# Performance work log

Hardware: AMD Instinct MI355X
Metric: run time of the kernel (lower is better)

## Reference

```python
import jax, jax.numpy as jnp
import numpy as np

KR = 2  # nb_row == stride_row
KC = 2  # nb_col == stride_col


def setup_inputs() -> dict:
    key = jax.random.key(0)
    k1, k2, k3 = jax.random.split(key, 3)
    B, C, H, W_ = 32, 32, 128, 128
    F = 64
    OR, OC = H // KR, W_ // KC
    x = jax.random.normal(k1, (B, C, H, W_), dtype=jnp.float32)
    W = jax.random.normal(k2, (F, C, H, W_), dtype=jnp.float32) * 0.05
    b = jax.random.normal(k3, (OR, OC, F), dtype=jnp.float32) * 0.05
    return {"x": x, "W": W, "b": b}


def reference(x, W, b):
    # x: (B, C, H, W), W: (F, C, H, W) -- unshared per-pixel weights
    # per-pixel channel contraction: (B, F, H, W)
    out = jnp.einsum('bchw,fchw->bfhw', x, W)
    B, F, H, Wd = out.shape
    OR, OC = H // KR, Wd // KC
    # stride*avg_pool == exact sum over non-overlapping (KR, KC) patches
    out = out.reshape(B, F, OR, KR, OC, KC).sum(axis=(3, 5))
    # keras does a RAW reshape of b from (OR, OC, F) to (1, F, OR, OC)
    out = out + b.reshape(1, F, OR, OC)
    return jax.nn.relu(out)
```

## Files before the change

kernel.cpp:

```cpp
#include <hip/hip_runtime.h>
#include <stdint.h>


#define CC  32
#define HH  128
#define WWD 128
#define FF  64
#define ORR 64
#define OCC 64
#define NIT 32
#define HW  (HH * WWD)
#define CHW (CC * HH * WWD)

__global__ __launch_bounds__(512, 4) void lc2d_kernel(
    const float* __restrict__ x, const float* __restrict__ wgt,
    const float* __restrict__ bias, float* __restrict__ out)
{
    __shared__ __align__(16) float Xs[4][2048];
    __shared__ __align__(16) float Ws[4][2048];

    const int tid  = threadIdx.x;
    const int id   = blockIdx.x;
    const int fblk = id >> 8;
    const int low  = id & 255;
    const int oct = ((low & 1) << 1) | (low >> 7);
    const int orr = (low >> 1) & 63;
    const int w0  = oct * 32;
    const int h0  = orr * 2;

    const int lane = tid & 63;
    const int wv   = tid >> 6;
    const int chk  = lane & 7;
    const int sub  = lane >> 3;

    const int skh = wv >> 2;
    const int bsw = sub * 4 + (wv & 3);
    const int flr = (wv & 3) * 8 + sub;
    const float* gx = x   + (((bsw * CC) * HH) + h0 + skh) * WWD + w0 + chk * 4;
    const float* gw = wgt + ((((fblk * 32 + flr) * CC) * HH) + h0 + skh) * WWD + w0 + chk * 4;

    auto issue = [&](int p) {
        __builtin_amdgcn_global_load_lds(
            (const __attribute__((address_space(1))) void*)gx,
            (__attribute__((address_space(3))) void*)(&Xs[p][wv * 256]), 16, 0, 0);
        __builtin_amdgcn_global_load_lds(
            (const __attribute__((address_space(1))) void*)gw,
            (__attribute__((address_space(3))) void*)(&Ws[p][wv * 256]), 16, 0, 0);
        gx += HW; gw += HW;
    };

    const int ocg = tid & 7;
    const int bg  = (tid >> 3) & 7;
    const int woff = wv * 128 + ocg * 4;

    float acc0[4][4], acc1[4][4];
#pragma unroll
    for (int i = 0; i < 4; ++i)
#pragma unroll
        for (int q = 0; q < 4; ++q) { acc0[i][q] = 0.f; acc1[i][q] = 0.f; }

    issue(0); issue(1); issue(2); issue(3);

    for (int it = 0; it < NIT; ++it) {
        const int rem = NIT - 1 - it;
        if (rem >= 3)      asm volatile("s_waitcnt vmcnt(6)");
        else if (rem == 2) asm volatile("s_waitcnt vmcnt(4)");
        else if (rem == 1) asm volatile("s_waitcnt vmcnt(2)");
        else               asm volatile("s_waitcnt vmcnt(0)");
        __builtin_amdgcn_sched_barrier(0);
        __builtin_amdgcn_s_barrier();
        __builtin_amdgcn_sched_barrier(0);

        const int p = it & 3;
        const float* Xp = Xs[p];
        const float* Wp = Ws[p];
#pragma unroll
        for (int s = 0; s < 2; ++s) {
            const float4* xr = (const float4*)(Xp + s * 1024 + (lane << 2));
            const float4* wr = (const float4*)(Wp + s * 1024 + woff);
            float4 xa[4], wb[4];
#pragma unroll
            for (int i = 0; i < 4; ++i) xa[i] = xr[i * 64];
#pragma unroll
            for (int q = 0; q < 4; ++q) wb[q] = wr[q * 8];
#pragma unroll
            for (int i = 0; i < 4; ++i)
#pragma unroll
                for (int q = 0; q < 4; ++q) {
                    acc0[i][q] = fmaf(xa[i].x, wb[q].x, acc0[i][q]);
                    acc0[i][q] = fmaf(xa[i].y, wb[q].y, acc0[i][q]);
                    acc1[i][q] = fmaf(xa[i].z, wb[q].z, acc1[i][q]);
                    acc1[i][q] = fmaf(xa[i].w, wb[q].w, acc1[i][q]);
                }
        }
        __builtin_amdgcn_sched_barrier(0);
        __builtin_amdgcn_s_barrier();
        __builtin_amdgcn_sched_barrier(0);
        if (it + 4 < NIT) issue(p);
    }

    const int oc0 = oct * 16 + ocg * 2;
#pragma unroll
    for (int q = 0; q < 4; ++q) {
        const int f = fblk * 32 + wv * 4 + q;
        const float2 bv = *(const float2*)(bias + f * (ORR * OCC) + orr * OCC + oc0);
#pragma unroll
        for (int i = 0; i < 4; ++i) {
            const int b = bg * 4 + i;
            float2 o;
            o.x = fmaxf(acc0[i][q] + bv.x, 0.f);
            o.y = fmaxf(acc1[i][q] + bv.y, 0.f);
            *(float2*)(out + (((b * FF + f) * ORR + orr) * OCC) + oc0) = o;
        }
    }
}

extern "C" void kernel_launch(void* const* d_in, const int* in_sizes, int n_in,
                              void* d_out, int out_size, void* d_ws, size_t ws_size,
                              hipStream_t stream) {
    (void)in_sizes; (void)n_in; (void)d_ws; (void)ws_size; (void)out_size;
    const float* x    = (const float*)d_in[0];
    const float* wgt  = (const float*)d_in[1];
    const float* bias = (const float*)d_in[2];
    float* out        = (float*)d_out;
    lc2d_kernel<<<dim3(512, 1, 1), dim3(512, 1, 1), 0, stream>>>(x, wgt, bias, out);
}
```

Baseline: 263.4 us.

## Replace LDS-staged async pipeline with direct global float4 loads per thread

Drops the four-stage shared-memory ring buffer fed by global_load_lds, along with its waitcnt and barrier synchronization. Each thread now reads its x and W float4 tiles straight from global memory inside a channel loop unrolled by two. This removes LDS traffic and block-wide barriers. In exchange, data reuse across threads depends on the caches rather than LDS, and there is no explicit prefetch to hide global latency.

```diff
diff --git a/kernel.cpp b/kernel.cpp
--- a/kernel.cpp
+++ b/kernel.cpp
@@ -8,7 +8,6 @@
 #define FF  64
 #define ORR 64
 #define OCC 64
-#define NIT 32
 #define HW  (HH * WWD)
 #define CHW (CC * HH * WWD)
 
@@ -16,9 +15,6 @@
     const float* __restrict__ x, const float* __restrict__ wgt,
     const float* __restrict__ bias, float* __restrict__ out)
 {
-    __shared__ __align__(16) float Xs[4][2048];
-    __shared__ __align__(16) float Ws[4][2048];
-
     const int tid  = threadIdx.x;
     const int id   = blockIdx.x;
     const int fblk = id >> 8;
@@ -28,30 +24,12 @@
     const int w0  = oct * 32;
     const int h0  = orr * 2;
 
-    const int lane = tid & 63;
-    const int wv   = tid >> 6;
-    const int chk  = lane & 7;
-    const int sub  = lane >> 3;
-
-    const int skh = wv >> 2;
-    const int bsw = sub * 4 + (wv & 3);
-    const int flr = (wv & 3) * 8 + sub;
-    const float* gx = x   + (((bsw * CC) * HH) + h0 + skh) * WWD + w0 + chk * 4;
-    const float* gw = wgt + ((((fblk * 32 + flr) * CC) * HH) + h0 + skh) * WWD + w0 + chk * 4;
-
-    auto issue = [&](int p) {
-        __builtin_amdgcn_global_load_lds(
-            (const __attribute__((address_space(1))) void*)gx,
-            (__attribute__((address_space(3))) void*)(&Xs[p][wv * 256]), 16, 0, 0);
-        __builtin_amdgcn_global_load_lds(
-            (const __attribute__((address_space(1))) void*)gw,
-            (__attribute__((address_space(3))) void*)(&Ws[p][wv * 256]), 16, 0, 0);
-        gx += HW; gw += HW;
-    };
-
     const int ocg = tid & 7;
     const int bg  = (tid >> 3) & 7;
-    const int woff = wv * 128 + ocg * 4;
+    const int wv  = tid >> 6;
+
+    const float* gx = x + (((size_t)(bg * 4) * CC) * HH + h0) * WWD + w0 + ocg * 4;
+    const float* gw = wgt + (((size_t)(fblk * 32 + wv * 4) * CC) * HH + h0) * WWD + w0 + ocg * 4;
 
     float acc0[4][4], acc1[4][4];
 #pragma unroll
@@ -59,30 +37,17 @@
 #pragma unroll
         for (int q = 0; q < 4; ++q) { acc0[i][q] = 0.f; acc1[i][q] = 0.f; }
 
-    issue(0); issue(1); issue(2); issue(3);
-
-    for (int it = 0; it < NIT; ++it) {
-        const int rem = NIT - 1 - it;
-        if (rem >= 3)      asm volatile("s_waitcnt vmcnt(6)");
-        else if (rem == 2) asm volatile("s_waitcnt vmcnt(4)");
-        else if (rem == 1) asm volatile("s_waitcnt vmcnt(2)");
-        else               asm volatile("s_waitcnt vmcnt(0)");
-        __builtin_amdgcn_sched_barrier(0);
-        __builtin_amdgcn_s_barrier();
-        __builtin_amdgcn_sched_barrier(0);
-
-        const int p = it & 3;
-        const float* Xp = Xs[p];
-        const float* Wp = Ws[p];
+#pragma unroll 2
+    for (int c = 0; c < CC; ++c) {
 #pragma unroll
         for (int s = 0; s < 2; ++s) {
-            const float4* xr = (const float4*)(Xp + s * 1024 + (lane << 2));
-            const float4* wr = (const float4*)(Wp + s * 1024 + woff);
             float4 xa[4], wb[4];
 #pragma unroll
-            for (int i = 0; i < 4; ++i) xa[i] = xr[i * 64];
+            for (int i = 0; i < 4; ++i)
+                xa[i] = *(const float4*)(gx + (size_t)i * CHW + s * WWD);
 #pragma unroll
-            for (int q = 0; q < 4; ++q) wb[q] = wr[q * 8];
+            for (int q = 0; q < 4; ++q)
+                wb[q] = *(const float4*)(gw + (size_t)q * CHW + s * WWD);
 #pragma unroll
             for (int i = 0; i < 4; ++i)
 #pragma unroll
@@ -93,10 +58,7 @@
                     acc1[i][q] = fmaf(xa[i].w, wb[q].w, acc1[i][q]);
                 }
         }
-        __builtin_amdgcn_sched_barrier(0);
-        __builtin_amdgcn_s_barrier();
-        __builtin_amdgcn_sched_barrier(0);
-        if (it + 4 < NIT) issue(p);
+        gx += HW; gw += HW;
     }
 
     const int oc0 = oct * 16 + ocg * 2;
```

Measured after the change: 335.3 us. 27.3% more time.

## Halve filters per block and switch to triple-buffered single-barrier pipeline

Applied to the files above, without the earlier changes.

Each block now computes 16 filters instead of 32, using 256 threads and 1024 blocks. LDS staging goes from four buffers to three, and each iteration uses one barrier instead of two: the refill for the next-next stage is issued right after the barrier. The aim is more blocks in flight for better latency hiding and less synchronisation. The cost is that each x tile is now loaded by twice as many blocks, which doubles x global traffic.

```diff
diff --git a/kernel.cpp b/kernel.cpp
--- a/kernel.cpp
+++ b/kernel.cpp
@@ -12,17 +12,17 @@
 #define HW  (HH * WWD)
 #define CHW (CC * HH * WWD)
 
-__global__ __launch_bounds__(512, 4) void lc2d_kernel(
+__global__ __launch_bounds__(256, 4) void lc2d_kernel(
     const float* __restrict__ x, const float* __restrict__ wgt,
     const float* __restrict__ bias, float* __restrict__ out)
 {
-    __shared__ __align__(16) float Xs[4][2048];
-    __shared__ __align__(16) float Ws[4][2048];
+    __shared__ __align__(16) float Xs[3][2048];
+    __shared__ __align__(16) float Ws[3][1024];
 
-    const int tid  = threadIdx.x;
-    const int id   = blockIdx.x;
-    const int fblk = id >> 8;
-    const int low  = id & 255;
+    const int tid = threadIdx.x;
+    const int id  = blockIdx.x;
+    const int fq  = id >> 8;
+    const int low = id & 255;
     const int oct = ((low & 1) << 1) | (low >> 7);
     const int orr = (low >> 1) & 63;
     const int w0  = oct * 32;
@@ -33,25 +33,36 @@
     const int chk  = lane & 7;
     const int sub  = lane >> 3;
 
-    const int skh = wv >> 2;
-    const int bsw = sub * 4 + (wv & 3);
-    const int flr = (wv & 3) * 8 + sub;
-    const float* gx = x   + (((bsw * CC) * HH) + h0 + skh) * WWD + w0 + chk * 4;
-    const float* gw = wgt + ((((fblk * 32 + flr) * CC) * HH) + h0 + skh) * WWD + w0 + chk * 4;
+    const float* gxA;
+    const float* gxB;
+    {
+        const int kA = wv * 2, kB = wv * 2 + 1;
+        const int bA = sub * 4 + (kA & 3), sA = kA >> 2;
+        const int bB = sub * 4 + (kB & 3), sB = kB >> 2;
+        gxA = x + (((bA * CC) * HH) + h0 + sA) * WWD + w0 + chk * 4;
+        gxB = x + (((bB * CC) * HH) + h0 + sB) * WWD + w0 + chk * 4;
+    }
+    const float* gw;
+    {
+        const int r = wv * 8 + sub;
+        gw = wgt + ((((fq * 16 + (r & 15)) * CC) * HH) + h0 + (r >> 4)) * WWD + w0 + chk * 4;
+    }
 
     auto issue = [&](int p) {
         __builtin_amdgcn_global_load_lds(
-            (const __attribute__((address_space(1))) void*)gx,
-            (__attribute__((address_space(3))) void*)(&Xs[p][wv * 256]), 16, 0, 0);
+            (const __attribute__((address_space(1))) void*)gxA,
+            (__attribute__((address_space(3))) void*)(&Xs[p][(wv * 2) * 256 + 0]), 16, 0, 0);
+        __builtin_amdgcn_global_load_lds(
+            (const __attribute__((address_space(1))) void*)gxB,
+            (__attribute__((address_space(3))) void*)(&Xs[p][(wv * 2 + 1) * 256]), 16, 0, 0);
         __builtin_amdgcn_global_load_lds(
             (const __attribute__((address_space(1))) void*)gw,
             (__attribute__((address_space(3))) void*)(&Ws[p][wv * 256]), 16, 0, 0);
-        gx += HW; gw += HW;
+        gxA += HW; gxB += HW; gw += HW;
     };
 
     const int ocg = tid & 7;
     const int bg  = (tid >> 3) & 7;
-    const int woff = wv * 128 + ocg * 4;
 
     float acc0[4][4], acc1[4][4];
 #pragma unroll
@@ -59,25 +70,27 @@
 #pragma unroll
         for (int q = 0; q < 4; ++q) { acc0[i][q] = 0.f; acc1[i][q] = 0.f; }
 
-    issue(0); issue(1); issue(2); issue(3);
+    issue(0); issue(1);
 
+    int p = 0;
     for (int it = 0; it < NIT; ++it) {
-        const int rem = NIT - 1 - it;
-        if (rem >= 3)      asm volatile("s_waitcnt vmcnt(6)");
-        else if (rem == 2) asm volatile("s_waitcnt vmcnt(4)");
-        else if (rem == 1) asm volatile("s_waitcnt vmcnt(2)");
-        else               asm volatile("s_waitcnt vmcnt(0)");
+        if (it < NIT - 1) asm volatile("s_waitcnt vmcnt(3)");
+        else              asm volatile("s_waitcnt vmcnt(0)");
         __builtin_amdgcn_sched_barrier(0);
         __builtin_amdgcn_s_barrier();
         __builtin_amdgcn_sched_barrier(0);
+        if (it + 2 < NIT) {
+            const int pn = (p + 2) % 3;
+            issue(pn);
+        }
+        __builtin_amdgcn_sched_barrier(0);
 
-        const int p = it & 3;
         const float* Xp = Xs[p];
         const float* Wp = Ws[p];
 #pragma unroll
         for (int s = 0; s < 2; ++s) {
             const float4* xr = (const float4*)(Xp + s * 1024 + (lane << 2));
-            const float4* wr = (const float4*)(Wp + s * 1024 + woff);
+            const float4* wr = (const float4*)(Wp + s * 512 + wv * 128 + ocg * 4);
             float4 xa[4], wb[4];
 #pragma unroll
             for (int i = 0; i < 4; ++i) xa[i] = xr[i * 64];
@@ -93,16 +106,13 @@
                     acc1[i][q] = fmaf(xa[i].w, wb[q].w, acc1[i][q]);
                 }
         }
-        __builtin_amdgcn_sched_barrier(0);
-        __builtin_amdgcn_s_barrier();
-        __builtin_amdgcn_sched_barrier(0);
-        if (it + 4 < NIT) issue(p);
+        p = (p + 1) % 3;
     }
 
     const int oc0 = oct * 16 + ocg * 2;
 #pragma unroll
     for (int q = 0; q < 4; ++q) {
-        const int f = fblk * 32 + wv * 4 + q;
+        const int f = fq * 16 + wv * 4 + q;
         const float2 bv = *(const float2*)(bias + f * (ORR * OCC) + orr * OCC + oc0);
 #pragma unroll
         for (int i = 0; i < 4; ++i) {
@@ -123,5 +133,5 @@
     const float* wgt  = (const float*)d_in[1];
     const float* bias = (const float*)d_in[2];
     float* out        = (float*)d_out;
-    lc2d_kernel<<<dim3(512, 1, 1), dim3(512, 1, 1), 0, stream>>>(x, wgt, bias, out);
+    lc2d_kernel<<<dim3(1024, 1, 1), dim3(256, 1, 1), 0, stream>>>(x, wgt, bias, out);
 }
```

New measurement: 272.5 us. 1.03x slower.
